# Performance work log

Hardware: AMD Instinct MI355X
Metric: run time of the kernel (lower is better)

## Reference

```python
import jax, jax.numpy as jnp
import numpy as np

BATCH, SEQ, HIDDEN = 8, 2048, 2048
N_FREQS = SEQ // 2 + 1  # 1025


def setup_inputs() -> dict:
    key = jax.random.key(0)
    k_x, k_w, k_b = jax.random.split(key, 3)
    x = jax.random.normal(k_x, (BATCH, SEQ, HIDDEN), dtype=jnp.float32)
    # Params per __init__: gate init ones/zeros; Linear(hidden, hidden)
    gate_real = jnp.ones((N_FREQS, HIDDEN), dtype=jnp.float32)
    gate_imag = jnp.zeros((N_FREQS, HIDDEN), dtype=jnp.float32)
    bound = 1.0 / np.sqrt(HIDDEN)
    W = jax.random.uniform(k_w, (HIDDEN, HIDDEN), minval=-bound, maxval=bound, dtype=jnp.float32)
    b = jax.random.uniform(k_b, (HIDDEN,), minval=-bound, maxval=bound, dtype=jnp.float32)
    return {"x": x, "gate_real": gate_real, "gate_imag": gate_imag, "W": W, "b": b}


def reference(x, gate_real, gate_imag, W, b):
    # x: (batch, seq, hidden)
    seq_len = x.shape[1]
    x_fft = jnp.fft.rfft(x, axis=1)  # (batch, n_freqs, hidden) complex64
    n_freqs = x_fft.shape[1]
    gate = gate_real[:n_freqs] + 1j * gate_imag[:n_freqs]  # (n_freqs, hidden)
    x_fft = x_fft * gate
    y = jnp.fft.irfft(x_fft, n=seq_len, axis=1)  # (batch, seq, hidden) float32
    # out_proj: y @ W.T + b  (torch Linear convention, W: (out, in))
    out = jnp.einsum('bsh,oh->bso', y, W) + b
    return out
```

## Files before the change

kernel.cpp:

```cpp
#include <hip/hip_runtime.h>
#include <math.h>

typedef __attribute__((ext_vector_type(8))) short bf16x8;
typedef __attribute__((ext_vector_type(4))) float f32x4;

__device__ __forceinline__ unsigned short f2bf(float f) {
  unsigned int u = __float_as_uint(f);
  unsigned int r = (u + 0x7fffu + ((u >> 16) & 1u)) >> 16;
  return (unsigned short)r;
}
__device__ __forceinline__ unsigned int pack2bf(float a, float b) {
  return (unsigned int)f2bf(a) | ((unsigned int)f2bf(b) << 16);
}
__device__ __forceinline__ float bflo(unsigned int g) { return __uint_as_float(g << 16); }
__device__ __forceinline__ float bfhi(unsigned int g) { return __uint_as_float(g & 0xffff0000u); }

__device__ __forceinline__ void glds16(const void* gp, void* lp) {
  __builtin_amdgcn_global_load_lds(
      (const __attribute__((address_space(1))) void*)gp,
      (__attribute__((address_space(3))) void*)lp, 16, 0, 0);
}

__device__ __constant__ float CW16[16] = {
  1.0f, 0.9807852804032304f, 0.9238795325112867f, 0.8314696123025452f,
  0.7071067811865476f, 0.5555702330196022f, 0.3826834323650898f, 0.19509032201612828f,
  0.0f, -0.19509032201612828f, -0.3826834323650898f, -0.5555702330196022f,
  -0.7071067811865476f, -0.8314696123025452f, -0.9238795325112867f, -0.9807852804032304f};
__device__ __constant__ float SW16[16] = {
  0.0f, 0.19509032201612828f, 0.3826834323650898f, 0.5555702330196022f,
  0.7071067811865476f, 0.8314696123025452f, 0.9238795325112867f, 0.9807852804032304f,
  1.0f, 0.9807852804032304f, 0.9238795325112867f, 0.8314696123025452f,
  0.7071067811865476f, 0.5555702330196022f, 0.3826834323650898f, 0.19509032201612828f};
__device__ __constant__ int BR5[32] = {
  0,16,8,24,4,20,12,28,2,18,10,26,6,22,14,30,
  1,17,9,25,5,21,13,29,3,19,11,27,7,23,15,31};

__device__ __forceinline__ int bitrev6(int l) {
  return ((l&1)<<5)|((l&2)<<3)|((l&4)<<1)|((l&8)>>1)|((l&16)>>3)|((l&32)>>5);
}

__device__ __forceinline__ float hsin(float rev) { return __builtin_amdgcn_sinf(rev); }
__device__ __forceinline__ float hcos(float rev) { return __builtin_amdgcn_cosf(rev); }

__device__ __forceinline__ void fwd_core(float (&ur)[32], float (&ui)[32], const int lane) {
  #pragma unroll
  for (int s = 0; s < 6; ++s) {
    const int h = 32 >> s;
    const int j = lane & (h - 1);
    const float rev = (float)j * (0.5f / (float)h);
    const bool hi = (lane & h) != 0;
    const float c  = hi ? hcos(rev) : 1.0f;
    const float sv = hi ? hsin(rev) : 0.0f;
    const float sgn = hi ? -1.0f : 1.0f;
    #pragma unroll
    for (int r = 0; r < 32; ++r) {
      float pr = __shfl_xor(ur[r], h, 64);
      float pi = __shfl_xor(ui[r], h, 64);
      float tr = fmaf(sgn, ur[r], pr);
      float ti = fmaf(sgn, ui[r], pi);
      ur[r] = fmaf(ti, sv, tr * c);
      ui[r] = fmaf(-tr, sv, ti * c);
    }
  }
  const int kap = bitrev6(lane);
  #pragma unroll
  for (int j = 1; j < 32; ++j) {
    const float rev = (float)(j * kap) * (1.0f / 2048.0f);
    const float sn = hsin(rev), cs = hcos(rev);
    float t = ur[j] * cs + ui[j] * sn;
    ui[j] = ui[j] * cs - ur[j] * sn;
    ur[j] = t;
  }
  #pragma unroll
  for (int s = 0; s < 5; ++s) {
    const int h = 16 >> s;
    #pragma unroll
    for (int i = 0; i < 32; ++i) if (!(i & h)) {
      const int tw = (i & (h - 1)) * (16 / h);
      float dr = ur[i] - ur[i + h], di = ui[i] - ui[i + h];
      ur[i] += ur[i + h]; ui[i] += ui[i + h];
      ur[i + h] = dr * CW16[tw] + di * SW16[tw];
      ui[i + h] = di * CW16[tw] - dr * SW16[tw];
    }
  }
}

__device__ __forceinline__ void inv_core(float (&ur)[32], float (&ui)[32], const int lane) {
  const int kap = bitrev6(lane);
  #pragma unroll
  for (int s = 0; s < 5; ++s) {
    const int h = 1 << s;
    #pragma unroll
    for (int i = 0; i < 32; ++i) if (!(i & h)) {
      const int tw = (i & (h - 1)) * (16 / h);
      float tr2 = ur[i + h] * CW16[tw] - ui[i + h] * SW16[tw];
      float ti2 = ui[i + h] * CW16[tw] + ur[i + h] * SW16[tw];
      ur[i + h] = ur[i] - tr2; ui[i + h] = ui[i] - ti2;
      ur[i] += tr2; ui[i] += ti2;
    }
  }
  #pragma unroll
  for (int j = 1; j < 32; ++j) {
    const float rev = (float)(j * kap) * (1.0f / 2048.0f);
    const float sn = hsin(rev), cs = hcos(rev);
    float t = ur[j] * cs - ui[j] * sn;
    ui[j] = ui[j] * cs + ur[j] * sn;
    ur[j] = t;
  }
  #pragma unroll
  for (int s = 0; s < 6; ++s) {
    const int h = 1 << s;
    const int j = lane & (h - 1);
    const float rev = (float)j * (0.5f / (float)h);
    const bool hi = (lane & h) != 0;
    const float c  = hi ? hcos(rev) : 1.0f;
    const float sv = hi ? hsin(rev) : 0.0f;
    const float sgn = hi ? -1.0f : 1.0f;
    #pragma unroll
    for (int r = 0; r < 32; ++r) {
      float vr = fmaf(-ui[r], sv, ur[r] * c);
      float vi = fmaf(ur[r], sv, ui[r] * c);
      float pvr = __shfl_xor(vr, h, 64);
      float pvi = __shfl_xor(vi, h, 64);
      ur[r] = fmaf(sgn, vr, pvr);
      ui[r] = fmaf(sgn, vi, pvi);
    }
  }
}

__global__ __launch_bounds__(256) void gate_pack_k(const float* __restrict__ gr,
                                                   const float* __restrict__ gi,
                                                   unsigned int* __restrict__ gt) {
  __shared__ float tr[32][33];
  __shared__ float ti[32][33];
  const int t = threadIdx.x;
  const int k0 = blockIdx.x * 32, hb = blockIdx.y * 32;
  const int hx = t & 31, fr = t >> 5;
  #pragma unroll
  for (int p = 0; p < 4; ++p) {
    int ff = p * 8 + fr;
    int k = k0 + ff;
    int f = (k <= 1024) ? k : (2048 - k);
    float sg = (k <= 1024) ? 1.f : -1.f;
    tr[ff][hx] = gr[(size_t)f * 2048 + hb + hx] * (1.f / 2048.f);
    ti[ff][hx] = sg * gi[(size_t)f * 2048 + hb + hx] * (1.f / 2048.f);
  }
  __syncthreads();
  const int kk = t & 31, hr = t >> 5;
  #pragma unroll
  for (int p = 0; p < 4; ++p) {
    int hl = p * 8 + hr;
    float re = tr[kk][hl], im = ti[kk][hl];
    gt[(size_t)(hb + hl) * 2048 + k0 + kk] =
        (unsigned int)f2bf(re) | ((unsigned int)f2bf(im) << 16);
  }
}

__global__ __launch_bounds__(256) void gate_ab_k(const float* __restrict__ gr,
                                                 const float* __restrict__ gi,
                                                 uint2* __restrict__ ab) {
  __shared__ unsigned int uA[32][33];
  __shared__ unsigned int uB[32][33];
  const int t = threadIdx.x;
  const int k0 = blockIdx.x * 32, h0 = blockIdx.y * 32;
  const int c = t & 31, r = t >> 5;
  #pragma unroll
  for (int pp = 0; pp < 4; ++pp) {
    const int kk = pp * 8 + r;
    const int k = k0 + kk;
    const int h = h0 + c;
    const float gkr = gr[(size_t)k * 2048 + h];
    const float gki = gi[(size_t)k * 2048 + h];
    const float gcr = gr[(size_t)(1024 - k) * 2048 + h];
    const float gci = gi[(size_t)(1024 - k) * 2048 + h];
    const float inv = 1.0f / 1024.0f;
    float Ar, Ai, Br, Bi;
    if (k == 0) {
      Ar = (gkr + gcr) * 0.5f * inv; Ai = 0.f;
      Br = 0.f; Bi = (gkr - gcr) * 0.5f * inv;
    } else {
      const float rev = (float)k * (1.0f / 2048.0f);
      const float sn = hsin(rev), cs = hcos(rev);
      const float Sr = (gkr + gcr) * 0.5f, Si = (gki - gci) * 0.5f;
      const float Dr = (gkr - gcr) * 0.5f, Di = (gki + gci) * 0.5f;
      Ar = (Sr - sn * Dr) * inv; Ai = (Si - sn * Di) * inv;
      Br = (-cs * Di) * inv;     Bi = (cs * Dr) * inv;
    }
    uA[kk][c] = pack2bf(Ar, Ai);
    uB[kk][c] = pack2bf(Br, Bi);
  }
  __syncthreads();
  #pragma unroll
  for (int pp = 0; pp < 4; ++pp) {
    const int hh = pp * 8 + r;
    ab[(size_t)(h0 + hh) * 1024 + k0 + c] = make_uint2(uA[c][hh], uB[c][hh]);
  }
}

__global__ __launch_bounds__(256) void wconv_k(const float* __restrict__ W,
                                               unsigned short* __restrict__ Wb) {
  int i = blockIdx.x * 256 + threadIdx.x;
  float4 v = ((const float4*)W)[i];
  ushort4 o;
  o.x = f2bf(v.x); o.y = f2bf(v.y); o.z = f2bf(v.z); o.w = f2bf(v.w);
  ((ushort4*)Wb)[i] = o;
}

__global__ __launch_bounds__(256) void xtrans_k(const float* __restrict__ x,
                                                float* __restrict__ xT) {
  __shared__ float t[32][33];
  const int b = blockIdx.z;
  const int s0 = blockIdx.x * 32, h0 = blockIdx.y * 32;
  const float* xb = x + ((size_t)b * 2048) * 2048;
  float* xTb = xT + ((size_t)b * 2048) * 2048;
  const int c = threadIdx.x & 31, r = threadIdx.x >> 5;
  #pragma unroll
  for (int p = 0; p < 4; ++p) {
    int rr = p * 8 + r;
    t[rr][c] = xb[(size_t)(s0 + rr) * 2048 + h0 + c];
  }
  __syncthreads();
  #pragma unroll
  for (int p = 0; p < 4; ++p) {
    int rr = p * 8 + r;
    xTb[(size_t)(h0 + rr) * 2048 + s0 + c] = t[c][rr];
  }
}

__global__ __launch_bounds__(256) void ytrans_k(const unsigned short* __restrict__ yT,
                                                unsigned short* __restrict__ y) {
  __shared__ unsigned short t[64][66];
  const int b = blockIdx.z;
  const int h0 = blockIdx.x * 64, s0 = blockIdx.y * 64;
  const unsigned short* src = yT + ((size_t)b * 2048 + h0) * 2048 + s0;
  unsigned short* dst = y + ((size_t)b * 2048 + s0) * 2048 + h0;
  const int c = threadIdx.x & 15, r = threadIdx.x >> 4;
  #pragma unroll
  for (int p = 0; p < 4; ++p) {
    int rr = p * 16 + r;
    ushort4 v = *(const ushort4*)(src + (size_t)rr * 2048 + c * 4);
    *(ushort4*)&t[rr][c * 4] = v;
  }
  __syncthreads();
  #pragma unroll
  for (int p = 0; p < 4; ++p) {
    int rr = p * 16 + r;
    ushort4 o;
    o.x = t[c * 4 + 0][rr]; o.y = t[c * 4 + 1][rr];
    o.z = t[c * 4 + 2][rr]; o.w = t[c * 4 + 3][rr];
    *(ushort4*)(dst + (size_t)rr * 2048 + c * 4) = o;
  }
}

__global__ __attribute__((amdgpu_flat_work_group_size(256, 256)))
__attribute__((amdgpu_waves_per_eu(2, 4)))
void fftr_k(const float* __restrict__ xT,
            const uint2* __restrict__ ab,
            unsigned short* __restrict__ yT) {
  __shared__ float snap[4][32];
  const int tid = threadIdx.x;
  const int w = tid >> 6, lane = tid & 63;
  const size_t col = (size_t)blockIdx.x * 4 + w;
  const int h = (int)(col & 2047);

  float ur[16], ui[16];
  const float4* xc = (const float4*)(xT + col * 2048);
  #pragma unroll
  for (int q = 0; q < 8; ++q) {
    float4 v = xc[lane * 8 + q];
    ur[2 * q]     = v.x; ui[2 * q]     = v.y;
    ur[2 * q + 1] = v.z; ui[2 * q + 1] = v.w;
  }

  #pragma unroll
  for (int s = 0; s < 6; ++s) {
    const int hh = 32 >> s;
    const int j = lane & (hh - 1);
    const float rev = (float)j * (0.5f / (float)hh);
    const bool hi = (lane & hh) != 0;
    const float c  = hi ? hcos(rev) : 1.0f;
    const float sv = hi ? hsin(rev) : 0.0f;
    const float sgn = hi ? -1.0f : 1.0f;
    #pragma unroll
    for (int r = 0; r < 16; ++r) {
      float pr = __shfl_xor(ur[r], hh, 64);
      float pi = __shfl_xor(ui[r], hh, 64);
      float tr = fmaf(sgn, ur[r], pr);
      float ti = fmaf(sgn, ui[r], pi);
      ur[r] = fmaf(ti, sv, tr * c);
      ui[r] = fmaf(-tr, sv, ti * c);
    }
  }
  const int kap = bitrev6(lane);
  #pragma unroll
  for (int j = 1; j < 16; ++j) {
    const float rev = (float)(j * kap) * (1.0f / 1024.0f);
    const float sn = hsin(rev), cs = hcos(rev);
    float t = ur[j] * cs + ui[j] * sn;
    ui[j] = ui[j] * cs - ur[j] * sn;
    ur[j] = t;
  }
  #pragma unroll
  for (int s = 0; s < 4; ++s) {
    const int hh = 8 >> s;
    #pragma unroll
    for (int i = 0; i < 16; ++i) if (!(i & hh)) {
      const int tw = (i & (hh - 1)) * (16 / hh);
      float dr = ur[i] - ur[i + hh], di = ui[i] - ui[i + hh];
      ur[i] += ur[i + hh]; ui[i] += ui[i + hh];
      ur[i + hh] = dr * CW16[tw] + di * SW16[tw];
      ui[i + hh] = di * CW16[tw] - dr * SW16[tw];
    }
  }

  if (lane == 0) {
    #pragma unroll
    for (int p = 0; p < 16; ++p) { snap[w][2 * p] = ur[p]; snap[w][2 * p + 1] = ui[p]; }
  }
  const int lsrc = bitrev6((64 - kap) & 63);
  const uint2* abrow = ab + (size_t)h * 1024;
  constexpr int BR4[16]   = {0,8,4,12,2,10,6,14,1,9,5,13,3,11,7,15};
  constexpr int P0L16[16] = {0,1,3,2,7,6,5,4,15,14,13,12,11,10,9,8};
  const bool l0 = (lane == 0);
  #pragma unroll
  for (int p = 0; p < 8; ++p) {
    const int pb = 15 - p;
    float arp = __shfl(ur[pb], lsrc), aip = __shfl(ui[pb], lsrc);
    float arq = __shfl(ur[p], lsrc),  aiq = __shfl(ui[p], lsrc);
    float s0r = snap[w][2 * P0L16[p]],  s0i = snap[w][2 * P0L16[p] + 1];
    float s1r = snap[w][2 * P0L16[pb]], s1i = snap[w][2 * P0L16[pb] + 1];
    arp = l0 ? s0r : arp;  aip = l0 ? s0i : aip;
    arq = l0 ? s1r : arq;  aiq = l0 ? s1i : aiq;
    uint2 gp = abrow[(BR4[p]  << 6) + kap];
    uint2 gq = abrow[(BR4[pb] << 6) + kap];
    {
      float Ar = bflo(gp.x), Ai = bfhi(gp.x), Br = bflo(gp.y), Bi = bfhi(gp.y);
      float zr = ur[p], zi = ui[p];
      ur[p] = Ar * zr - Ai * zi + Br * arp + Bi * aip;
      ui[p] = Ar * zi + Ai * zr + Bi * arp - Br * aip;
    }
    {
      float Ar = bflo(gq.x), Ai = bfhi(gq.x), Br = bflo(gq.y), Bi = bfhi(gq.y);
      float zr = ur[pb], zi = ui[pb];
      ur[pb] = Ar * zr - Ai * zi + Br * arq + Bi * aiq;
      ui[pb] = Ar * zi + Ai * zr + Bi * arq - Br * aiq;
    }
  }

  #pragma unroll
  for (int s = 0; s < 4; ++s) {
    const int hh = 1 << s;
    #pragma unroll
    for (int i = 0; i < 16; ++i) if (!(i & hh)) {
      const int tw = (i & (hh - 1)) * (16 / hh);
      float tr2 = ur[i + hh] * CW16[tw] - ui[i + hh] * SW16[tw];
      float ti2 = ui[i + hh] * CW16[tw] + ur[i + hh] * SW16[tw];
      ur[i + hh] = ur[i] - tr2; ui[i + hh] = ui[i] - ti2;
      ur[i] += tr2; ui[i] += ti2;
    }
  }
  #pragma unroll
  for (int j = 1; j < 16; ++j) {
    const float rev = (float)(j * kap) * (1.0f / 1024.0f);
    const float sn = hsin(rev), cs = hcos(rev);
    float t = ur[j] * cs - ui[j] * sn;
    ui[j] = ui[j] * cs + ur[j] * sn;
    ur[j] = t;
  }
  #pragma unroll
  for (int s = 0; s < 6; ++s) {
    const int hh = 1 << s;
    const int j = lane & (hh - 1);
    const float rev = (float)j * (0.5f / (float)hh);
    const bool hi = (lane & hh) != 0;
    const float c  = hi ? hcos(rev) : 1.0f;
    const float sv = hi ? hsin(rev) : 0.0f;
    const float sgn = hi ? -1.0f : 1.0f;
    #pragma unroll
    for (int r = 0; r < 16; ++r) {
      float vr = fmaf(-ui[r], sv, ur[r] * c);
      float vi = fmaf(ur[r], sv, ui[r] * c);
      float pvr = __shfl_xor(vr, hh, 64);
      float pvi = __shfl_xor(vi, hh, 64);
      ur[r] = fmaf(sgn, vr, pvr);
      ui[r] = fmaf(sgn, vi, pvi);
    }
  }

  uint4* dst = (uint4*)(yT + col * 2048) + lane * 4;
  #pragma unroll
  for (int g = 0; g < 4; ++g) {
    uint4 o;
    o.x = pack2bf(ur[4 * g + 0], ui[4 * g + 0]);
    o.y = pack2bf(ur[4 * g + 1], ui[4 * g + 1]);
    o.z = pack2bf(ur[4 * g + 2], ui[4 * g + 2]);
    o.w = pack2bf(ur[4 * g + 3], ui[4 * g + 3]);
    dst[g] = o;
  }
}

__global__ __attribute__((amdgpu_flat_work_group_size(512, 512)))
__attribute__((amdgpu_waves_per_eu(2, 4)))
void fft_gate_k(const float* __restrict__ x,
                const unsigned int* __restrict__ gt,
                unsigned short* __restrict__ y) {
  __shared__ float lds[8 * 516];
  const int tid = threadIdx.x;
  const int w = tid >> 6;
  const int lane = tid & 63;
  const int bid = blockIdx.x;
  const int swz = (bid & 7) * 256 + (bid >> 3);
  const int h0 = (swz & 255) << 3;
  const int b = swz >> 8;
  const int hh = tid & 7, srow = tid >> 3;

  float ur[32], ui[32];
  const size_t xbase = ((size_t)b * 2048) * 2048 + h0;

  for (int c = 0; c < 4; ++c) {
    #pragma unroll
    for (int q = 0; q < 8; ++q) {
      int soff = q * 64 + srow;
      float v = x[xbase + (size_t)(c * 512 + soff) * 2048 + hh];
      lds[hh * 516 + (soff ^ ((soff >> 5) & 15))] = v;
    }
    __syncthreads();
    if ((lane >> 4) == c) {
      const int li = lane & 15;
      #pragma unroll
      for (int j = 0; j < 32; ++j) {
        ur[j] = lds[w * 516 + ((32 * li + j) ^ li)];
        ui[j] = 0.f;
      }
    }
    __syncthreads();
  }

  fwd_core(ur, ui, lane);
  {
    const int kap = bitrev6(lane);
    const unsigned int* grow = gt + (size_t)(h0 + w) * 2048;
    #pragma unroll
    for (int p = 0; p < 32; ++p) {
      unsigned int g = grow[(BR5[p] << 6) + kap];
      float gre = bflo(g), gim = bfhi(g);
      float t = ur[p] * gre - ui[p] * gim;
      ui[p] = ur[p] * gim + ui[p] * gre;
      ur[p] = t;
    }
  }
  inv_core(ur, ui, lane);

  for (int c = 0; c < 4; ++c) {
    if ((lane >> 4) == c) {
      const int li = lane & 15;
      #pragma unroll
      for (int r = 0; r < 32; ++r)
        lds[w * 516 + ((32 * li + r) ^ li)] = ur[r];
    }
    __syncthreads();
    #pragma unroll
    for (int q = 0; q < 8; ++q) {
      int soff = q * 64 + srow;
      float v = lds[hh * 516 + (soff ^ ((soff >> 5) & 15))];
      y[xbase + (size_t)(c * 512 + soff) * 2048 + hh] = f2bf(v);
    }
    __syncthreads();
  }
}

__global__ __launch_bounds__(256) void gemm_k(const unsigned short* __restrict__ A,
                                              const unsigned short* __restrict__ Bw,
                                              const float* __restrict__ bias,
                                              float* __restrict__ C) {
  __shared__ unsigned short sA[128 * 32];
  __shared__ unsigned short sB[128 * 32];
  const int tid = threadIdx.x;
  const int nwg = gridDim.x;
  const int cpx = nwg >> 3;
  const int bid = blockIdx.x;
  const int swz = (bid & 7) * cpx + (bid >> 3);
  const int bm = swz >> 4, bn = swz & 15;
  const int m0 = bm << 7, n0 = bn << 7;
  const int w = tid >> 6, lane = tid & 63;
  const int arow = tid >> 2, koff = (tid & 3) << 3;
  const unsigned short* gA = A + (size_t)(m0 + arow) * 2048 + koff;
  const unsigned short* gB = Bw + (size_t)(n0 + arow) * 2048 + koff;
  char* sAb = (char*)sA + w * 1024;
  char* sBb = (char*)sB + w * 1024;

  f32x4 acc[4][4];
  #pragma unroll
  for (int i = 0; i < 4; ++i)
    #pragma unroll
    for (int j = 0; j < 4; ++j) acc[i][j] = (f32x4){0.f, 0.f, 0.f, 0.f};

  const int wr = w >> 1, wc = w & 1;
  const int row16 = lane & 15, kb = lane >> 4;

  for (int k0 = 0; k0 < 2048; k0 += 32) {
    glds16(gA + k0, sAb);
    glds16(gA + 64 * 2048 + k0, sAb + 4096);
    glds16(gB + k0, sBb);
    glds16(gB + 64 * 2048 + k0, sBb + 4096);
    __syncthreads();
    bf16x8 af[4], bfr[4];
    #pragma unroll
    for (int i = 0; i < 4; ++i) {
      int r = (wr << 6) + (i << 4) + row16;
      af[i] = *(const bf16x8*)(sA + r * 32 + (kb << 3));
    }
    #pragma unroll
    for (int j2 = 0; j2 < 4; ++j2) {
      int r = (wc << 6) + (j2 << 4) + row16;
      bfr[j2] = *(const bf16x8*)(sB + r * 32 + (kb << 3));
    }
    #pragma unroll
    for (int i = 0; i < 4; ++i)
      #pragma unroll
      for (int j2 = 0; j2 < 4; ++j2)
        acc[i][j2] = __builtin_amdgcn_mfma_f32_16x16x32_bf16(af[i], bfr[j2], acc[i][j2], 0, 0, 0);
    __syncthreads();
  }

  const int rq = lane >> 4;
  #pragma unroll
  for (int j2 = 0; j2 < 4; ++j2) {
    int oc = n0 + (wc << 6) + (j2 << 4) + row16;
    float bj = bias[oc];
    #pragma unroll
    for (int i = 0; i < 4; ++i) {
      int mr = m0 + (wr << 6) + (i << 4) + (rq << 2);
      #pragma unroll
      for (int q = 0; q < 4; ++q)
        C[(size_t)(mr + q) * 2048 + oc] = acc[i][j2][q] + bj;
    }
  }
}

__global__ __launch_bounds__(512) void gemm8_k(const unsigned short* __restrict__ A,
                                               const unsigned short* __restrict__ Bw,
                                               const float* __restrict__ bias,
                                               float* __restrict__ C) {
  extern __shared__ char lds[];
  const int tid = threadIdx.x;
  const int w = tid >> 6, lane = tid & 63;
  const int bid = blockIdx.x;
  const int swz = (bid & 7) * 64 + (bid >> 3);
  const int m0 = (swz >> 3) << 8;
  const int n0 = (swz & 7) << 8;
  const int wr = w >> 2, wc = w & 3;
  const int row16 = lane & 15, kb = lane >> 4;

  const int lr = lane >> 2, ls = lane & 3;
  const int r0 = (w << 5) + lr, r1 = r0 + 16;
  const unsigned short* pA0 = A  + (size_t)(m0 + r0) * 2048 + ((ls ^ ((r0 >> 1) & 3)) << 3);
  const unsigned short* pA1 = A  + (size_t)(m0 + r1) * 2048 + ((ls ^ ((r1 >> 1) & 3)) << 3);
  const unsigned short* pB0 = Bw + (size_t)(n0 + r0) * 2048 + ((ls ^ ((r0 >> 1) & 3)) << 3);
  const unsigned short* pB1 = Bw + (size_t)(n0 + r1) * 2048 + ((ls ^ ((r1 >> 1) & 3)) << 3);
  const int dW = w << 11;

  f32x4 acc[8][4];
  #pragma unroll
  for (int i = 0; i < 8; ++i)
    #pragma unroll
    for (int j = 0; j < 4; ++j) acc[i][j] = (f32x4){0.f, 0.f, 0.f, 0.f};

  auto STAGE = [&](int t) {
    char* base = lds + ((t & 3) << 15);
    const int k0 = t << 5;
    glds16(pA0 + k0, base + dW);
    glds16(pA1 + k0, base + dW + 1024);
    glds16(pB0 + k0, base + 16384 + dW);
    glds16(pB1 + k0, base + 16384 + dW + 1024);
  };
  auto COMPUTE = [&](int t) {
    const char* base = lds + ((t & 3) << 15);
    bf16x8 af[8], bfr[4];
    #pragma unroll
    for (int i = 0; i < 8; ++i) {
      const int r = (wr << 7) + (i << 4) + row16;
      af[i] = *(const bf16x8*)(base + (r << 6) + ((kb ^ ((r >> 1) & 3)) << 4));
    }
    #pragma unroll
    for (int j = 0; j < 4; ++j) {
      const int r = (wc << 6) + (j << 4) + row16;
      bfr[j] = *(const bf16x8*)(base + 16384 + (r << 6) + ((kb ^ ((r >> 1) & 3)) << 4));
    }
    #pragma unroll
    for (int i = 0; i < 8; ++i)
      #pragma unroll
      for (int j = 0; j < 4; ++j)
        acc[i][j] = __builtin_amdgcn_mfma_f32_16x16x32_bf16(af[i], bfr[j], acc[i][j], 0, 0, 0);
  };

  STAGE(0); STAGE(1); STAGE(2);
  asm volatile("s_waitcnt vmcnt(8)" ::: "memory");
  __builtin_amdgcn_s_barrier();
  __builtin_amdgcn_sched_barrier(0);

  for (int t = 0; t < 61; ++t) {
    STAGE(t + 3);
    COMPUTE(t);
    asm volatile("s_waitcnt vmcnt(8)" ::: "memory");
    __builtin_amdgcn_s_barrier();
    __builtin_amdgcn_sched_barrier(0);
  }
  COMPUTE(61);
  asm volatile("s_waitcnt vmcnt(4)" ::: "memory");
  __builtin_amdgcn_s_barrier();
  __builtin_amdgcn_sched_barrier(0);
  COMPUTE(62);
  asm volatile("s_waitcnt vmcnt(0)" ::: "memory");
  __builtin_amdgcn_s_barrier();
  __builtin_amdgcn_sched_barrier(0);
  COMPUTE(63);

  const int rq = lane >> 4;
  #pragma unroll
  for (int j = 0; j < 4; ++j) {
    const int oc = n0 + (wc << 6) + (j << 4) + row16;
    const float bj = bias[oc];
    #pragma unroll
    for (int i = 0; i < 8; ++i) {
      const int mr = m0 + (wr << 7) + (i << 4) + (rq << 2);
      #pragma unroll
      for (int q = 0; q < 4; ++q)
        C[(size_t)(mr + q) * 2048 + oc] = acc[i][j][q] + bj;
    }
  }
}

extern "C" void kernel_launch(void* const* d_in, const int* in_sizes, int n_in,
                              void* d_out, int out_size, void* d_ws, size_t ws_size,
                              hipStream_t stream) {
  const float* x  = (const float*)d_in[0];
  const float* gr = (const float*)d_in[1];
  const float* gi = (const float*)d_in[2];
  const float* W  = (const float*)d_in[3];
  const float* bs = (const float*)d_in[4];
  float* out = (float*)d_out;

  char* ws = (char*)d_ws;
  unsigned short* yb = (unsigned short*)ws;
  unsigned short* Wb = (unsigned short*)(ws + (64ull << 20));
  unsigned int*   gt = (unsigned int*)(ws + (72ull << 20));
  uint2*          ab = (uint2*)(ws + (72ull << 20));
  float*          xT = (float*)(ws + (88ull << 20));
  unsigned short* yT = (unsigned short*)(ws + (216ull << 20));
  const bool fast = ws_size >= (280ull << 20);

  hipLaunchKernelGGL(wconv_k, dim3(4096), dim3(256), 0, stream, W, Wb);
  if (fast) {
    hipLaunchKernelGGL(gate_ab_k, dim3(32, 64), dim3(256), 0, stream, gr, gi, ab);
    hipLaunchKernelGGL(xtrans_k, dim3(64, 64, 8), dim3(256), 0, stream, x, xT);
    hipLaunchKernelGGL(fftr_k, dim3(4096), dim3(256), 0, stream, xT, ab, yT);
    hipLaunchKernelGGL(ytrans_k, dim3(32, 32, 8), dim3(256), 0, stream, yT, yb);
  } else {
    hipLaunchKernelGGL(gate_pack_k, dim3(64, 64), dim3(256), 0, stream, gr, gi, gt);
    hipLaunchKernelGGL(fft_gate_k, dim3(2048), dim3(512), 0, stream, x, gt, yb);
  }

  const bool big = hipFuncSetAttribute((const void*)gemm8_k,
                                       hipFuncAttributeMaxDynamicSharedMemorySize,
                                       131072) == hipSuccess;
  if (big) {
    hipLaunchKernelGGL(gemm8_k, dim3(512), dim3(512), 131072, stream, yb, Wb, bs, out);
  } else {
    hipLaunchKernelGGL(gemm_k, dim3(2048), dim3(256), 0, stream, yb, Wb, bs, out);
  }
}
```

Baseline: 373.9 us.

## Split GEMM main loop into two phases interleaving LDS reads, global loads and MFMA

```diff
diff --git a/kernel.cpp b/kernel.cpp
--- a/kernel.cpp
+++ b/kernel.cpp
@@ -566,42 +566,71 @@
     #pragma unroll
     for (int j = 0; j < 4; ++j) acc[i][j] = (f32x4){0.f, 0.f, 0.f, 0.f};
 
-  auto STAGE = [&](int t) {
+  auto STAGE_A = [&](int t) {
     char* base = lds + ((t & 3) << 15);
     const int k0 = t << 5;
     glds16(pA0 + k0, base + dW);
     glds16(pA1 + k0, base + dW + 1024);
+  };
+  auto STAGE_B = [&](int t) {
+    char* base = lds + ((t & 3) << 15);
+    const int k0 = t << 5;
     glds16(pB0 + k0, base + 16384 + dW);
     glds16(pB1 + k0, base + 16384 + dW + 1024);
   };
-  auto COMPUTE = [&](int t) {
-    const char* base = lds + ((t & 3) << 15);
-    bf16x8 af[8], bfr[4];
-    #pragma unroll
-    for (int i = 0; i < 8; ++i) {
-      const int r = (wr << 7) + (i << 4) + row16;
+  auto LDA4 = [&](const char* base, int i0, bf16x8 (&af)[4]) {
+    #pragma unroll
+    for (int i = 0; i < 4; ++i) {
+      const int r = (wr << 7) + ((i0 + i) << 4) + row16;
       af[i] = *(const bf16x8*)(base + (r << 6) + ((kb ^ ((r >> 1) & 3)) << 4));
     }
+  };
+  auto LDB4 = [&](const char* base, bf16x8 (&bfr)[4]) {
     #pragma unroll
     for (int j = 0; j < 4; ++j) {
       const int r = (wc << 6) + (j << 4) + row16;
       bfr[j] = *(const bf16x8*)(base + 16384 + (r << 6) + ((kb ^ ((r >> 1) & 3)) << 4));
     }
-    #pragma unroll
-    for (int i = 0; i < 8; ++i)
+  };
+  auto MM16 = [&](const bf16x8 (&af)[4], const bf16x8 (&bfr)[4], int i0) {
+    #pragma unroll
+    for (int i = 0; i < 4; ++i)
       #pragma unroll
       for (int j = 0; j < 4; ++j)
-        acc[i][j] = __builtin_amdgcn_mfma_f32_16x16x32_bf16(af[i], bfr[j], acc[i][j], 0, 0, 0);
+        acc[i0 + i][j] = __builtin_amdgcn_mfma_f32_16x16x32_bf16(af[i], bfr[j], acc[i0 + i][j], 0, 0, 0);
   };
-
-  STAGE(0); STAGE(1); STAGE(2);
+  auto COMPUTE = [&](int t) {
+    const char* base = lds + ((t & 3) << 15);
+    bf16x8 af[4], af2[4], bfr[4];
+    LDA4(base, 0, af); LDA4(base, 4, af2); LDB4(base, bfr);
+    MM16(af, bfr, 0); MM16(af2, bfr, 4);
+  };
+
+  STAGE_A(0); STAGE_B(0); STAGE_A(1); STAGE_B(1); STAGE_A(2); STAGE_B(2);
   asm volatile("s_waitcnt vmcnt(8)" ::: "memory");
   __builtin_amdgcn_s_barrier();
   __builtin_amdgcn_sched_barrier(0);
 
   for (int t = 0; t < 61; ++t) {
-    STAGE(t + 3);
-    COMPUTE(t);
+    const char* base = lds + ((t & 3) << 15);
+    bf16x8 af[4], bfr[4];
+    LDA4(base, 0, af);
+    LDB4(base, bfr);
+    STAGE_A(t + 3);
+    asm volatile("s_waitcnt lgkmcnt(0)" ::: "memory");
+    __builtin_amdgcn_sched_barrier(0);
+    __builtin_amdgcn_s_setprio(1);
+    MM16(af, bfr, 0);
+    __builtin_amdgcn_s_setprio(0);
+    __builtin_amdgcn_s_barrier();
+    bf16x8 af2[4];
+    LDA4(base, 4, af2);
+    STAGE_B(t + 3);
+    asm volatile("s_waitcnt lgkmcnt(0)" ::: "memory");
+    __builtin_amdgcn_sched_barrier(0);
+    __builtin_amdgcn_s_setprio(1);
+    MM16(af2, bfr, 4);
+    __builtin_amdgcn_s_setprio(0);
     asm volatile("s_waitcnt vmcnt(8)" ::: "memory");
     __builtin_amdgcn_s_barrier();
     __builtin_amdgcn_sched_barrier(0);
```

New measurement: 366.9 us. About the same (-1.9%).
